# Optimization experiments

Measured on AMD Instinct MI355X. Metric: run time of the kernel, lower is better.

Reference implementation:

```python
import jax, jax.numpy as jnp
import numpy as np

OUTPUT_LEN = 180  # decoder steps, from __init__ default


def gru_cell(x, h, Wih, Whh, bih, bhh):
    """PyTorch-convention GRU cell. x:(B,in) h:(B,H) -> (B,H)."""
    gi = x @ Wih.T + bih          # (B,3H)
    gh = h @ Whh.T + bhh          # (B,3H)
    ir, iz, inn = jnp.split(gi, 3, axis=-1)
    hr, hz, hn = jnp.split(gh, 3, axis=-1)
    r = jax.nn.sigmoid(ir + hr)
    z = jax.nn.sigmoid(iz + hz)
    n = jnp.tanh(inn + r * hn)
    return (1.0 - z) * n + z * h


def setup_inputs() -> dict:
    key = jax.random.key(0)
    B, T_in, N_IN, H = 8192, 512, 2, 64
    ks = jax.random.split(key, 20)
    s = 0.05
    d = {
        "x": jax.random.normal(ks[0], (B, T_in, N_IN), jnp.float32),
        "enc_Wih0": jax.random.normal(ks[1], (3 * H, N_IN), jnp.float32) * s,
        "enc_Whh0": jax.random.normal(ks[2], (3 * H, H), jnp.float32) * s,
        "enc_bih0": jax.random.normal(ks[3], (3 * H,), jnp.float32) * s,
        "enc_bhh0": jax.random.normal(ks[4], (3 * H,), jnp.float32) * s,
        "enc_Wih1": jax.random.normal(ks[5], (3 * H, H), jnp.float32) * s,
        "enc_Whh1": jax.random.normal(ks[6], (3 * H, H), jnp.float32) * s,
        "enc_bih1": jax.random.normal(ks[7], (3 * H,), jnp.float32) * s,
        "enc_bhh1": jax.random.normal(ks[8], (3 * H,), jnp.float32) * s,
        "dec_Wih0": jax.random.normal(ks[9], (3 * H, 1), jnp.float32) * s,
        "dec_Whh0": jax.random.normal(ks[10], (3 * H, H), jnp.float32) * s,
        "dec_bih0": jax.random.normal(ks[11], (3 * H,), jnp.float32) * s,
        "dec_bhh0": jax.random.normal(ks[12], (3 * H,), jnp.float32) * s,
        "dec_Wih1": jax.random.normal(ks[13], (3 * H, H), jnp.float32) * s,
        "dec_Whh1": jax.random.normal(ks[14], (3 * H, H), jnp.float32) * s,
        "dec_bih1": jax.random.normal(ks[15], (3 * H,), jnp.float32) * s,
        "dec_bhh1": jax.random.normal(ks[16], (3 * H,), jnp.float32) * s,
        "out_W": jax.random.normal(ks[17], (1, H), jnp.float32) * s,
        "out_b": jax.random.normal(ks[18], (1,), jnp.float32) * s,
    }
    return d


def reference(x, enc_Wih0, enc_Whh0, enc_bih0, enc_bhh0,
              enc_Wih1, enc_Whh1, enc_bih1, enc_bhh1,
              dec_Wih0, dec_Whh0, dec_bih0, dec_bhh0,
              dec_Wih1, dec_Whh1, dec_bih1, dec_bhh1,
              out_W, out_b):
    B = x.shape[0]
    H = enc_Whh0.shape[1]
    h0 = jnp.zeros((B, H), x.dtype)
    h1 = jnp.zeros((B, H), x.dtype)

    # ---- encoder: 2-layer GRU over input_len steps ----
    def enc_step(carry, xt):
        h0, h1 = carry
        h0 = gru_cell(xt, h0, enc_Wih0, enc_Whh0, enc_bih0, enc_bhh0)
        h1 = gru_cell(h0, h1, enc_Wih1, enc_Whh1, enc_bih1, enc_bhh1)
        return (h0, h1), None

    (h0, h1), _ = jax.lax.scan(enc_step, (h0, h1), jnp.swapaxes(x, 0, 1))

    prev = jnp.zeros((B, 1), x.dtype)

    def dec_step(carry, _):
        h0, h1, prev = carry
        h0 = gru_cell(prev, h0, dec_Wih0, dec_Whh0, dec_bih0, dec_bhh0)
        h1 = gru_cell(h0, h1, dec_Wih1, dec_Whh1, dec_bih1, dec_bhh1)
        cv = h1 @ out_W.T + out_b          # (B,1)
        return (h0, h1, cv), cv

    _, ys = jax.lax.scan(dec_step, (h0, h1, prev), None, length=OUTPUT_LEN)
    # ys: (T, B, 1) -> (B, T, 1)
    return jnp.swapaxes(ys, 0, 1)
```

## Files before the change

kernel.cpp:

```cpp
#include <hip/hip_runtime.h>


typedef __attribute__((ext_vector_type(8))) short bf16x8;
typedef __attribute__((ext_vector_type(4))) float f32x4;

struct Params {
  const float *x;
  const float *wih0e, *bih0e, *bhh0e, *bih1e, *bhh1e;
  const float *wih0d, *bih0d, *bhh0d, *bih1d, *bhh1d;
  const float *outW, *outb;
  const unsigned short *wt;
  float *out;
};

__device__ __forceinline__ float sgm(float v) { return 1.f / (1.f + __expf(-v)); }
__device__ __forceinline__ float th(float v)  { float e = __expf(2.f * v); return 1.f - 2.f / (e + 1.f); }

__device__ __forceinline__ unsigned short rbf(float v) {
  unsigned int u = __float_as_uint(v);
  return (unsigned short)((u + 0x7fffu + ((u >> 16) & 1u)) >> 16);
}
__device__ __forceinline__ float ubf(unsigned short h) {
  return __uint_as_float((unsigned int)h << 16);
}

__device__ __forceinline__ f32x4 mfma16(bf16x8 a, bf16x8 b, f32x4 c) {
  return __builtin_amdgcn_mfma_f32_16x16x32_bf16(a, b, c, 0, 0, 0);
}

__global__ void prep_w(const float* s0, const float* s1, const float* s2,
                       const float* s3, const float* s4, const float* s5,
                       unsigned short* dst) {
  const float* srcs[6] = {s0, s1, s2, s3, s4, s5};
  const float* s = srcs[blockIdx.x];
  unsigned short* o = dst + blockIdx.x * 24576;
  for (int i = threadIdx.x; i < 24576; i += blockDim.x) {
    int e  = i & 7;
    int l  = (i >> 3) & 63;
    int sp = (i >> 9) & 1;
    int kf = (i >> 10) & 1;
    int nt = i >> 11;
    int n = nt * 16 + (l & 15);
    int k = kf * 32 + (l >> 4) * 8 + e;
    float v = s[n * 64 + k];
    unsigned short hi = rbf(v);
    unsigned short val = hi;
    if (sp) val = rbf(v - ubf(hi));
    o[i] = val;
  }
}


__global__ __launch_bounds__(256, 2) void gru_main(Params p) {
  __shared__ unsigned short aH0[2][2048];
  __shared__ unsigned short aH1[2][2048];
  __shared__ float pw[4][16];

  const int tid = threadIdx.x;
  const int l   = tid & 63;
  const int w   = tid >> 6;
  const int jc  = l & 15;
  const int rg  = l >> 4;
  const int j   = w * 16 + jc;
  const int b0  = blockIdx.x * 16;

  const int kfj = j >> 5, rgj = (j >> 3) & 3, ej = j & 7;
  const int wbase = kfj * 1024 + rgj * 128 + ej;
  const int rdb = rg * 128 + ((jc ^ rg) << 3);

  for (int i = tid; i < 2048; i += 256) {
    aH0[0][i] = 0; aH0[1][i] = 0; aH1[0][i] = 0; aH1[1][i] = 0;
  }
  float h0own[4] = {0.f, 0.f, 0.f, 0.f}, h1own[4] = {0.f, 0.f, 0.f, 0.f};

  bf16x8 wB[3][3][2][2];

  for (int ph = 0; ph < 2; ++ph) {
#pragma unroll
    for (int m = 0; m < 3; ++m)
#pragma unroll
      for (int g = 0; g < 3; ++g)
#pragma unroll
        for (int kf = 0; kf < 2; ++kf)
#pragma unroll
          for (int sp = 0; sp < 2; ++sp) {
            int nt = g * 4 + w;
            wB[m][g][kf][sp] = *(const bf16x8*)(p.wt +
                (((((ph * 3 + m) * 12 + nt) * 2 + kf) * 2 + sp) << 9) + l * 8);
          }
    float bi0[3], bh0[3], bi1[3], bh1[3], wxa[3], wxb[3];
#pragma unroll
    for (int g = 0; g < 3; ++g) {
      int r = g * 64 + j;
      if (ph == 0) {
        bi0[g] = p.bih0e[r]; bh0[g] = p.bhh0e[r];
        bi1[g] = p.bih1e[r]; bh1[g] = p.bhh1e[r];
        wxa[g] = p.wih0e[2 * r]; wxb[g] = p.wih0e[2 * r + 1];
      } else {
        bi0[g] = p.bih0d[r]; bh0[g] = p.bhh0d[r];
        bi1[g] = p.bih1d[r]; bh1[g] = p.bhh1d[r];
        wxa[g] = p.wih0d[r]; wxb[g] = 0.f;
      }
    }
    const float oW = p.outW[j], ob = p.outb[0];
    const int T = ph ? 180 : 512;
    __syncthreads();

    for (int t = 0; t < T; ++t) {
#pragma unroll
      for (int m = 0; m < 3; ++m)
#pragma unroll
        for (int g = 0; g < 3; ++g)
#pragma unroll
          for (int kf = 0; kf < 2; ++kf)
#pragma unroll
            for (int sp = 0; sp < 2; ++sp)
              asm volatile("" : "+v"(wB[m][g][kf][sp]));

      const int cur = t & 1;
      float2 xx[4]; float prevv[4];
      if (ph == 0) {
#pragma unroll
        for (int i = 0; i < 4; ++i)
          xx[i] = *(const float2*)(p.x + ((size_t)(b0 + rg * 4 + i) * 512 + t) * 2);
      } else {
        if (t > 0) {
#pragma unroll
          for (int i = 0; i < 4; ++i)
            prevv[i] = ob + pw[0][rg * 4 + i] + pw[1][rg * 4 + i]
                          + pw[2][rg * 4 + i] + pw[3][rg * 4 + i];
          if (w == 0 && jc == 0) {
#pragma unroll
            for (int i = 0; i < 4; ++i)
              p.out[(size_t)(b0 + rg * 4 + i) * 180 + (t - 1)] = prevv[i];
          }
        } else {
#pragma unroll
          for (int i = 0; i < 4; ++i) prevv[i] = 0.f;
        }
      }
      const unsigned short* h0o = aH0[cur ^ 1];
      f32x4 aR = {0,0,0,0}, aZ = {0,0,0,0}, aN = {0,0,0,0};
#pragma unroll
      for (int kf = 0; kf < 2; ++kf) {
        bf16x8 ah = *(const bf16x8*)&h0o[kf * 1024 + rdb];
        bf16x8 al = *(const bf16x8*)&h0o[kf * 1024 + 512 + rdb];
        aR = mfma16(ah, wB[0][0][kf][0], aR);
        aZ = mfma16(ah, wB[0][1][kf][0], aZ);
        aN = mfma16(ah, wB[0][2][kf][0], aN);
        aR = mfma16(al, wB[0][0][kf][0], aR);
        aZ = mfma16(al, wB[0][1][kf][0], aZ);
        aN = mfma16(al, wB[0][2][kf][0], aN);
        aR = mfma16(ah, wB[0][0][kf][1], aR);
        aZ = mfma16(ah, wB[0][1][kf][1], aZ);
        aN = mfma16(ah, wB[0][2][kf][1], aN);
      }
      unsigned short* h0n = aH0[cur];
#pragma unroll
      for (int i = 0; i < 4; ++i) {
        float xr, xz, xn;
        if (ph == 0) {
          xr = bi0[0] + wxa[0] * xx[i].x + wxb[0] * xx[i].y;
          xz = bi0[1] + wxa[1] * xx[i].x + wxb[1] * xx[i].y;
          xn = bi0[2] + wxa[2] * xx[i].x + wxb[2] * xx[i].y;
        } else {
          xr = bi0[0] + wxa[0] * prevv[i];
          xz = bi0[1] + wxa[1] * prevv[i];
          xn = bi0[2] + wxa[2] * prevv[i];
        }
        float r = sgm(xr + bh0[0] + aR[i]);
        float z = sgm(xz + bh0[1] + aZ[i]);
        float n = th(xn + r * (bh0[2] + aN[i]));
        h0own[i] = (1.f - z) * n + z * h0own[i];
        unsigned short hi = rbf(h0own[i]);
        unsigned short lo = rbf(h0own[i] - ubf(hi));
        int idx = wbase + (((rg * 4 + i) ^ rgj) << 3);
        h0n[idx] = hi; h0n[idx + 512] = lo;
      }
      __syncthreads();
      const unsigned short* h1o = aH1[cur ^ 1];
      f32x4 cR = {0,0,0,0}, cZ = {0,0,0,0}, iN = {0,0,0,0}, hN = {0,0,0,0};
#pragma unroll
      for (int kf = 0; kf < 2; ++kf) {
        bf16x8 gh = *(const bf16x8*)&h0n[kf * 1024 + rdb];
        bf16x8 gl = *(const bf16x8*)&h0n[kf * 1024 + 512 + rdb];
        bf16x8 qh = *(const bf16x8*)&h1o[kf * 1024 + rdb];
        bf16x8 ql = *(const bf16x8*)&h1o[kf * 1024 + 512 + rdb];
        cR = mfma16(gh, wB[1][0][kf][0], cR);
        cR = mfma16(qh, wB[2][0][kf][0], cR);
        cZ = mfma16(gh, wB[1][1][kf][0], cZ);
        cZ = mfma16(qh, wB[2][1][kf][0], cZ);
        iN = mfma16(gh, wB[1][2][kf][0], iN);
        hN = mfma16(qh, wB[2][2][kf][0], hN);
        cR = mfma16(gl, wB[1][0][kf][0], cR);
        cR = mfma16(ql, wB[2][0][kf][0], cR);
        cZ = mfma16(gl, wB[1][1][kf][0], cZ);
        cZ = mfma16(ql, wB[2][1][kf][0], cZ);
        iN = mfma16(gl, wB[1][2][kf][0], iN);
        hN = mfma16(ql, wB[2][2][kf][0], hN);
        cR = mfma16(gh, wB[1][0][kf][1], cR);
        cR = mfma16(qh, wB[2][0][kf][1], cR);
        cZ = mfma16(gh, wB[1][1][kf][1], cZ);
        cZ = mfma16(qh, wB[2][1][kf][1], cZ);
        iN = mfma16(gh, wB[1][2][kf][1], iN);
        hN = mfma16(qh, wB[2][2][kf][1], hN);
      }
      unsigned short* h1n = aH1[cur];
      float v[4];
#pragma unroll
      for (int i = 0; i < 4; ++i) {
        float r = sgm(cR[i] + bi1[0] + bh1[0]);
        float z = sgm(cZ[i] + bi1[1] + bh1[1]);
        float n = th(iN[i] + bi1[2] + r * (bh1[2] + hN[i]));
        h1own[i] = (1.f - z) * n + z * h1own[i];
        unsigned short hi = rbf(h1own[i]);
        unsigned short lo = rbf(h1own[i] - ubf(hi));
        int idx = wbase + (((rg * 4 + i) ^ rgj) << 3);
        h1n[idx] = hi; h1n[idx + 512] = lo;
        v[i] = oW * h1own[i];
      }
      if (ph == 1) {
#pragma unroll
        for (int off = 1; off < 16; off <<= 1)
#pragma unroll
          for (int i = 0; i < 4; ++i) v[i] += __shfl_xor(v[i], off, 64);
        if (jc == 0) {
#pragma unroll
          for (int i = 0; i < 4; ++i) pw[w][rg * 4 + i] = v[i];
        }
      }
      __syncthreads();
    }
    if (ph == 1) {
      if (w == 0 && jc == 0) {
#pragma unroll
        for (int i = 0; i < 4; ++i) {
          float fv = ob + pw[0][rg * 4 + i] + pw[1][rg * 4 + i]
                        + pw[2][rg * 4 + i] + pw[3][rg * 4 + i];
          p.out[(size_t)(b0 + rg * 4 + i) * 180 + 179] = fv;
        }
      }
    }
  }
}

extern "C" void kernel_launch(void* const* d_in, const int* in_sizes, int n_in,
                              void* d_out, int out_size, void* d_ws, size_t ws_size,
                              hipStream_t stream) {
  unsigned short* wt = (unsigned short*)d_ws;

  prep_w<<<dim3(6), dim3(256), 0, stream>>>(
      (const float*)d_in[2], (const float*)d_in[5], (const float*)d_in[6],
      (const float*)d_in[10], (const float*)d_in[13], (const float*)d_in[14], wt);

  Params p;
  p.x = (const float*)d_in[0];
  p.wih0e = (const float*)d_in[1];
  p.bih0e = (const float*)d_in[3];
  p.bhh0e = (const float*)d_in[4];
  p.bih1e = (const float*)d_in[7];
  p.bhh1e = (const float*)d_in[8];
  p.wih0d = (const float*)d_in[9];
  p.bih0d = (const float*)d_in[11];
  p.bhh0d = (const float*)d_in[12];
  p.bih1d = (const float*)d_in[15];
  p.bhh1d = (const float*)d_in[16];
  p.outW = (const float*)d_in[17];
  p.outb = (const float*)d_in[18];
  p.wt = wt;
  p.out = (float*)d_out;

  gru_main<<<dim3(512), dim3(256), 0, stream>>>(p);
}
```

Measured before the change: 2.159 ms.

## Process two 16-row batch tiles per block to reuse register-resident weights

Each block now handles 32 batch rows as two 16-row sub-tiles, so the weight fragments held in registers serve twice as many MFMAs. The grid halves to 256 blocks, about one per CU, and the layer-1 recurrent loads are hoisted ahead of the layer-0 MFMAs. The weight fragments are pinned to AGPRs with the "+a" constraint and the occupancy hint is dropped from launch_bounds. The aim is to amortize per-step barriers, LDS traffic and fixed latency over more work and to interleave independent MFMA chains. In exchange it roughly doubles live state per thread and lowers wave occupancy, which may reduce latency hiding.

Measured after the change: 2.534 ms. 17.4% more time.

```diff
diff --git a/kernel.cpp b/kernel.cpp
--- a/kernel.cpp
+++ b/kernel.cpp
@@ -51,10 +51,10 @@
 }
 
 
-__global__ __launch_bounds__(256, 2) void gru_main(Params p) {
-  __shared__ unsigned short aH0[2][2048];
-  __shared__ unsigned short aH1[2][2048];
-  __shared__ float pw[4][16];
+__global__ __launch_bounds__(256) void gru_main(Params p) {
+  __shared__ unsigned short aH0[2 * 4096];
+  __shared__ unsigned short aH1[2 * 4096];
+  __shared__ float pw[4][32];
 
   const int tid = threadIdx.x;
   const int l   = tid & 63;
@@ -62,16 +62,18 @@
   const int jc  = l & 15;
   const int rg  = l >> 4;
   const int j   = w * 16 + jc;
-  const int b0  = blockIdx.x * 16;
+  const int b0  = blockIdx.x * 32;
 
   const int kfj = j >> 5, rgj = (j >> 3) & 3, ej = j & 7;
   const int wbase = kfj * 1024 + rgj * 128 + ej;
   const int rdb = rg * 128 + ((jc ^ rg) << 3);
 
-  for (int i = tid; i < 2048; i += 256) {
-    aH0[0][i] = 0; aH0[1][i] = 0; aH1[0][i] = 0; aH1[1][i] = 0;
-  }
-  float h0own[4] = {0.f, 0.f, 0.f, 0.f}, h1own[4] = {0.f, 0.f, 0.f, 0.f};
+  for (int i = tid; i < 8192; i += 256) { aH0[i] = 0; aH1[i] = 0; }
+  float h0own[2][4], h1own[2][4];
+#pragma unroll
+  for (int rb = 0; rb < 2; ++rb)
+#pragma unroll
+    for (int i = 0; i < 4; ++i) { h0own[rb][i] = 0.f; h1own[rb][i] = 0.f; }
 
   bf16x8 wB[3][3][2][2];
 
@@ -115,118 +117,191 @@
           for (int kf = 0; kf < 2; ++kf)
 #pragma unroll
             for (int sp = 0; sp < 2; ++sp)
-              asm volatile("" : "+v"(wB[m][g][kf][sp]));
+              asm volatile("" : "+a"(wB[m][g][kf][sp]));
 
       const int cur = t & 1;
-      float2 xx[4]; float prevv[4];
+      const unsigned short* h0o = aH0 + (cur ^ 1) * 4096;
+      const unsigned short* h1o = aH1 + (cur ^ 1) * 4096;
+      unsigned short* h0n = aH0 + cur * 4096;
+      unsigned short* h1n = aH1 + cur * 4096;
+
+      float2 xx[2][4]; float prevv[2][4];
       if (ph == 0) {
 #pragma unroll
-        for (int i = 0; i < 4; ++i)
-          xx[i] = *(const float2*)(p.x + ((size_t)(b0 + rg * 4 + i) * 512 + t) * 2);
+        for (int rb = 0; rb < 2; ++rb)
+#pragma unroll
+          for (int i = 0; i < 4; ++i)
+            xx[rb][i] = *(const float2*)(p.x +
+                ((size_t)(b0 + rb * 16 + rg * 4 + i) * 512 + t) * 2);
       } else {
         if (t > 0) {
 #pragma unroll
-          for (int i = 0; i < 4; ++i)
-            prevv[i] = ob + pw[0][rg * 4 + i] + pw[1][rg * 4 + i]
-                          + pw[2][rg * 4 + i] + pw[3][rg * 4 + i];
+          for (int rb = 0; rb < 2; ++rb)
+#pragma unroll
+            for (int i = 0; i < 4; ++i) {
+              int b = rb * 16 + rg * 4 + i;
+              prevv[rb][i] = ob + pw[0][b] + pw[1][b] + pw[2][b] + pw[3][b];
+            }
           if (w == 0 && jc == 0) {
 #pragma unroll
-            for (int i = 0; i < 4; ++i)
-              p.out[(size_t)(b0 + rg * 4 + i) * 180 + (t - 1)] = prevv[i];
+            for (int rb = 0; rb < 2; ++rb)
+#pragma unroll
+              for (int i = 0; i < 4; ++i)
+                p.out[(size_t)(b0 + rb * 16 + rg * 4 + i) * 180 + (t - 1)] =
+                    prevv[rb][i];
           }
         } else {
 #pragma unroll
-          for (int i = 0; i < 4; ++i) prevv[i] = 0.f;
-        }
-      }
-      const unsigned short* h0o = aH0[cur ^ 1];
-      f32x4 aR = {0,0,0,0}, aZ = {0,0,0,0}, aN = {0,0,0,0};
+          for (int rb = 0; rb < 2; ++rb)
+#pragma unroll
+            for (int i = 0; i < 4; ++i) prevv[rb][i] = 0.f;
+        }
+      }
+
+      bf16x8 ah[2][2], al[2][2], qh[2][2], ql[2][2];
+#pragma unroll
+      for (int kf = 0; kf < 2; ++kf)
+#pragma unroll
+        for (int rb = 0; rb < 2; ++rb) {
+          ah[kf][rb] = *(const bf16x8*)&h0o[rb * 2048 + kf * 1024 + rdb];
+          al[kf][rb] = *(const bf16x8*)&h0o[rb * 2048 + kf * 1024 + 512 + rdb];
+          qh[kf][rb] = *(const bf16x8*)&h1o[rb * 2048 + kf * 1024 + rdb];
+          ql[kf][rb] = *(const bf16x8*)&h1o[rb * 2048 + kf * 1024 + 512 + rdb];
+        }
+
+      f32x4 aR[2], aZ[2], aN[2];
+#pragma unroll
+      for (int rb = 0; rb < 2; ++rb) {
+        f32x4 zz = {0.f, 0.f, 0.f, 0.f};
+        aR[rb] = zz; aZ[rb] = zz; aN[rb] = zz;
+      }
 #pragma unroll
       for (int kf = 0; kf < 2; ++kf) {
-        bf16x8 ah = *(const bf16x8*)&h0o[kf * 1024 + rdb];
-        bf16x8 al = *(const bf16x8*)&h0o[kf * 1024 + 512 + rdb];
-        aR = mfma16(ah, wB[0][0][kf][0], aR);
-        aZ = mfma16(ah, wB[0][1][kf][0], aZ);
-        aN = mfma16(ah, wB[0][2][kf][0], aN);
-        aR = mfma16(al, wB[0][0][kf][0], aR);
-        aZ = mfma16(al, wB[0][1][kf][0], aZ);
-        aN = mfma16(al, wB[0][2][kf][0], aN);
-        aR = mfma16(ah, wB[0][0][kf][1], aR);
-        aZ = mfma16(ah, wB[0][1][kf][1], aZ);
-        aN = mfma16(ah, wB[0][2][kf][1], aN);
-      }
-      unsigned short* h0n = aH0[cur];
-#pragma unroll
-      for (int i = 0; i < 4; ++i) {
-        float xr, xz, xn;
-        if (ph == 0) {
-          xr = bi0[0] + wxa[0] * xx[i].x + wxb[0] * xx[i].y;
-          xz = bi0[1] + wxa[1] * xx[i].x + wxb[1] * xx[i].y;
-          xn = bi0[2] + wxa[2] * xx[i].x + wxb[2] * xx[i].y;
-        } else {
-          xr = bi0[0] + wxa[0] * prevv[i];
-          xz = bi0[1] + wxa[1] * prevv[i];
-          xn = bi0[2] + wxa[2] * prevv[i];
-        }
-        float r = sgm(xr + bh0[0] + aR[i]);
-        float z = sgm(xz + bh0[1] + aZ[i]);
-        float n = th(xn + r * (bh0[2] + aN[i]));
-        h0own[i] = (1.f - z) * n + z * h0own[i];
-        unsigned short hi = rbf(h0own[i]);
-        unsigned short lo = rbf(h0own[i] - ubf(hi));
-        int idx = wbase + (((rg * 4 + i) ^ rgj) << 3);
-        h0n[idx] = hi; h0n[idx + 512] = lo;
-      }
+#pragma unroll
+        for (int rb = 0; rb < 2; ++rb) {
+          aR[rb] = mfma16(ah[kf][rb], wB[0][0][kf][0], aR[rb]);
+          aZ[rb] = mfma16(ah[kf][rb], wB[0][1][kf][0], aZ[rb]);
+          aN[rb] = mfma16(ah[kf][rb], wB[0][2][kf][0], aN[rb]);
+        }
+#pragma unroll
+        for (int rb = 0; rb < 2; ++rb) {
+          aR[rb] = mfma16(al[kf][rb], wB[0][0][kf][0], aR[rb]);
+          aZ[rb] = mfma16(al[kf][rb], wB[0][1][kf][0], aZ[rb]);
+          aN[rb] = mfma16(al[kf][rb], wB[0][2][kf][0], aN[rb]);
+        }
+#pragma unroll
+        for (int rb = 0; rb < 2; ++rb) {
+          aR[rb] = mfma16(ah[kf][rb], wB[0][0][kf][1], aR[rb]);
+          aZ[rb] = mfma16(ah[kf][rb], wB[0][1][kf][1], aZ[rb]);
+          aN[rb] = mfma16(ah[kf][rb], wB[0][2][kf][1], aN[rb]);
+        }
+      }
+#pragma unroll
+      for (int rb = 0; rb < 2; ++rb)
+#pragma unroll
+        for (int i = 0; i < 4; ++i) {
+          float xr, xz, xn;
+          if (ph == 0) {
+            xr = bi0[0] + wxa[0] * xx[rb][i].x + wxb[0] * xx[rb][i].y;
+            xz = bi0[1] + wxa[1] * xx[rb][i].x + wxb[1] * xx[rb][i].y;
+            xn = bi0[2] + wxa[2] * xx[rb][i].x + wxb[2] * xx[rb][i].y;
+          } else {
+            xr = bi0[0] + wxa[0] * prevv[rb][i];
+            xz = bi0[1] + wxa[1] * prevv[rb][i];
+            xn = bi0[2] + wxa[2] * prevv[rb][i];
+          }
+          float r = sgm(xr + bh0[0] + aR[rb][i]);
+          float z = sgm(xz + bh0[1] + aZ[rb][i]);
+          float n = th(xn + r * (bh0[2] + aN[rb][i]));
+          h0own[rb][i] = (1.f - z) * n + z * h0own[rb][i];
+          unsigned short hi = rbf(h0own[rb][i]);
+          unsigned short lo = rbf(h0own[rb][i] - ubf(hi));
+          int idx = rb * 2048 + wbase + (((rg * 4 + i) ^ rgj) << 3);
+          h0n[idx] = hi; h0n[idx + 512] = lo;
+        }
       __syncthreads();
-      const unsigned short* h1o = aH1[cur ^ 1];
-      f32x4 cR = {0,0,0,0}, cZ = {0,0,0,0}, iN = {0,0,0,0}, hN = {0,0,0,0};
+      bf16x8 gh[2][2], gl[2][2];
+#pragma unroll
+      for (int kf = 0; kf < 2; ++kf)
+#pragma unroll
+        for (int rb = 0; rb < 2; ++rb) {
+          gh[kf][rb] = *(const bf16x8*)&h0n[rb * 2048 + kf * 1024 + rdb];
+          gl[kf][rb] = *(const bf16x8*)&h0n[rb * 2048 + kf * 1024 + 512 + rdb];
+        }
+      f32x4 cR[2], cZ[2], iN2[2], hN2[2];
+#pragma unroll
+      for (int rb = 0; rb < 2; ++rb) {
+        f32x4 zz = {0.f, 0.f, 0.f, 0.f};
+        cR[rb] = zz; cZ[rb] = zz; iN2[rb] = zz; hN2[rb] = zz;
+      }
 #pragma unroll
       for (int kf = 0; kf < 2; ++kf) {
-        bf16x8 gh = *(const bf16x8*)&h0n[kf * 1024 + rdb];
-        bf16x8 gl = *(const bf16x8*)&h0n[kf * 1024 + 512 + rdb];
-        bf16x8 qh = *(const bf16x8*)&h1o[kf * 1024 + rdb];
-        bf16x8 ql = *(const bf16x8*)&h1o[kf * 1024 + 512 + rdb];
-        cR = mfma16(gh, wB[1][0][kf][0], cR);
-        cR = mfma16(qh, wB[2][0][kf][0], cR);
-        cZ = mfma16(gh, wB[1][1][kf][0], cZ);
-        cZ = mfma16(qh, wB[2][1][kf][0], cZ);
-        iN = mfma16(gh, wB[1][2][kf][0], iN);
-        hN = mfma16(qh, wB[2][2][kf][0], hN);
-        cR = mfma16(gl, wB[1][0][kf][0], cR);
-        cR = mfma16(ql, wB[2][0][kf][0], cR);
-        cZ = mfma16(gl, wB[1][1][kf][0], cZ);
-        cZ = mfma16(ql, wB[2][1][kf][0], cZ);
-        iN = mfma16(gl, wB[1][2][kf][0], iN);
-        hN = mfma16(ql, wB[2][2][kf][0], hN);
-        cR = mfma16(gh, wB[1][0][kf][1], cR);
-        cR = mfma16(qh, wB[2][0][kf][1], cR);
-        cZ = mfma16(gh, wB[1][1][kf][1], cZ);
-        cZ = mfma16(qh, wB[2][1][kf][1], cZ);
-        iN = mfma16(gh, wB[1][2][kf][1], iN);
-        hN = mfma16(qh, wB[2][2][kf][1], hN);
-      }
-      unsigned short* h1n = aH1[cur];
-      float v[4];
-#pragma unroll
-      for (int i = 0; i < 4; ++i) {
-        float r = sgm(cR[i] + bi1[0] + bh1[0]);
-        float z = sgm(cZ[i] + bi1[1] + bh1[1]);
-        float n = th(iN[i] + bi1[2] + r * (bh1[2] + hN[i]));
-        h1own[i] = (1.f - z) * n + z * h1own[i];
-        unsigned short hi = rbf(h1own[i]);
-        unsigned short lo = rbf(h1own[i] - ubf(hi));
-        int idx = wbase + (((rg * 4 + i) ^ rgj) << 3);
-        h1n[idx] = hi; h1n[idx + 512] = lo;
-        v[i] = oW * h1own[i];
-      }
+#pragma unroll
+        for (int rb = 0; rb < 2; ++rb) {
+          cR[rb]  = mfma16(gh[kf][rb], wB[1][0][kf][0], cR[rb]);
+          cZ[rb]  = mfma16(gh[kf][rb], wB[1][1][kf][0], cZ[rb]);
+          iN2[rb] = mfma16(gh[kf][rb], wB[1][2][kf][0], iN2[rb]);
+        }
+#pragma unroll
+        for (int rb = 0; rb < 2; ++rb) {
+          cR[rb]  = mfma16(qh[kf][rb], wB[2][0][kf][0], cR[rb]);
+          cZ[rb]  = mfma16(qh[kf][rb], wB[2][1][kf][0], cZ[rb]);
+          hN2[rb] = mfma16(qh[kf][rb], wB[2][2][kf][0], hN2[rb]);
+        }
+#pragma unroll
+        for (int rb = 0; rb < 2; ++rb) {
+          cR[rb]  = mfma16(gl[kf][rb], wB[1][0][kf][0], cR[rb]);
+          cZ[rb]  = mfma16(gl[kf][rb], wB[1][1][kf][0], cZ[rb]);
+          iN2[rb] = mfma16(gl[kf][rb], wB[1][2][kf][0], iN2[rb]);
+        }
+#pragma unroll
+        for (int rb = 0; rb < 2; ++rb) {
+          cR[rb]  = mfma16(ql[kf][rb], wB[2][0][kf][0], cR[rb]);
+          cZ[rb]  = mfma16(ql[kf][rb], wB[2][1][kf][0], cZ[rb]);
+          hN2[rb] = mfma16(ql[kf][rb], wB[2][2][kf][0], hN2[rb]);
+        }
+#pragma unroll
+        for (int rb = 0; rb < 2; ++rb) {
+          cR[rb]  = mfma16(gh[kf][rb], wB[1][0][kf][1], cR[rb]);
+          cZ[rb]  = mfma16(gh[kf][rb], wB[1][1][kf][1], cZ[rb]);
+          iN2[rb] = mfma16(gh[kf][rb], wB[1][2][kf][1], iN2[rb]);
+        }
+#pragma unroll
+        for (int rb = 0; rb < 2; ++rb) {
+          cR[rb]  = mfma16(qh[kf][rb], wB[2][0][kf][1], cR[rb]);
+          cZ[rb]  = mfma16(qh[kf][rb], wB[2][1][kf][1], cZ[rb]);
+          hN2[rb] = mfma16(qh[kf][rb], wB[2][2][kf][1], hN2[rb]);
+        }
+      }
+      float v[2][4];
+#pragma unroll
+      for (int rb = 0; rb < 2; ++rb)
+#pragma unroll
+        for (int i = 0; i < 4; ++i) {
+          float r = sgm(cR[rb][i] + bi1[0] + bh1[0]);
+          float z = sgm(cZ[rb][i] + bi1[1] + bh1[1]);
+          float n = th(iN2[rb][i] + bi1[2] + r * (bh1[2] + hN2[rb][i]));
+          h1own[rb][i] = (1.f - z) * n + z * h1own[rb][i];
+          unsigned short hi = rbf(h1own[rb][i]);
+          unsigned short lo = rbf(h1own[rb][i] - ubf(hi));
+          int idx = rb * 2048 + wbase + (((rg * 4 + i) ^ rgj) << 3);
+          h1n[idx] = hi; h1n[idx + 512] = lo;
+          v[rb][i] = oW * h1own[rb][i];
+        }
       if (ph == 1) {
 #pragma unroll
         for (int off = 1; off < 16; off <<= 1)
 #pragma unroll
-          for (int i = 0; i < 4; ++i) v[i] += __shfl_xor(v[i], off, 64);
+          for (int rb = 0; rb < 2; ++rb)
+#pragma unroll
+            for (int i = 0; i < 4; ++i)
+              v[rb][i] += __shfl_xor(v[rb][i], off, 64);
         if (jc == 0) {
 #pragma unroll
-          for (int i = 0; i < 4; ++i) pw[w][rg * 4 + i] = v[i];
+          for (int rb = 0; rb < 2; ++rb)
+#pragma unroll
+            for (int i = 0; i < 4; ++i)
+              pw[w][rb * 16 + rg * 4 + i] = v[rb][i];
         }
       }
       __syncthreads();
@@ -234,11 +309,13 @@
     if (ph == 1) {
       if (w == 0 && jc == 0) {
 #pragma unroll
-        for (int i = 0; i < 4; ++i) {
-          float fv = ob + pw[0][rg * 4 + i] + pw[1][rg * 4 + i]
-                        + pw[2][rg * 4 + i] + pw[3][rg * 4 + i];
-          p.out[(size_t)(b0 + rg * 4 + i) * 180 + 179] = fv;
-        }
+        for (int rb = 0; rb < 2; ++rb)
+#pragma unroll
+          for (int i = 0; i < 4; ++i) {
+            int b = rb * 16 + rg * 4 + i;
+            float fv = ob + pw[0][b] + pw[1][b] + pw[2][b] + pw[3][b];
+            p.out[(size_t)(b0 + b) * 180 + 179] = fv;
+          }
       }
     }
   }
@@ -270,5 +347,5 @@
   p.wt = wt;
   p.out = (float*)d_out;
 
-  gru_main<<<dim3(512), dim3(256), 0, stream>>>(p);
-}
+  gru_main<<<dim3(256), dim3(256), 0, stream>>>(p);
+}
```

## Stream layer-0 weights per step, pin layer-1 weights in AGPRs, hoist LDS reads

Applied to the files above, without the earlier changes.

Layer-0 recurrent weight fragments are no longer held in registers for the whole phase. They are reloaded from global memory (likely L1/L2 hits) every timestep, which cuts the resident weight register footprint by a third. The layer-1 weight fragments are now constrained to accumulator registers (AGPRs) via the asm constraint, freeing VGPRs. The previous-step h0/h1 LDS reads are hoisted ahead of the first MFMA chain and the MFMA order is interleaved. This trades extra global/cache traffic on the serial critical path for lower register pressure and possibly better scheduling.

After: 2.467 ms. +14.3%, slower.

```diff
diff --git a/kernel.cpp b/kernel.cpp
--- a/kernel.cpp
+++ b/kernel.cpp
@@ -73,11 +73,12 @@
   }
   float h0own[4] = {0.f, 0.f, 0.f, 0.f}, h1own[4] = {0.f, 0.f, 0.f, 0.f};
 
-  bf16x8 wB[3][3][2][2];
+  bf16x8 wB1[2][3][2][2];
 
   for (int ph = 0; ph < 2; ++ph) {
-#pragma unroll
-    for (int m = 0; m < 3; ++m)
+    const unsigned short* wt0 = p.wt + (ph * 3) * 24576;
+#pragma unroll
+    for (int m = 0; m < 2; ++m)
 #pragma unroll
       for (int g = 0; g < 3; ++g)
 #pragma unroll
@@ -85,8 +86,8 @@
 #pragma unroll
           for (int sp = 0; sp < 2; ++sp) {
             int nt = g * 4 + w;
-            wB[m][g][kf][sp] = *(const bf16x8*)(p.wt +
-                (((((ph * 3 + m) * 12 + nt) * 2 + kf) * 2 + sp) << 9) + l * 8);
+            wB1[m][g][kf][sp] = *(const bf16x8*)(p.wt +
+                (((((ph * 3 + 1 + m) * 12 + nt) * 2 + kf) * 2 + sp) << 9) + l * 8);
           }
     float bi0[3], bh0[3], bi1[3], bh1[3], wxa[3], wxb[3];
 #pragma unroll
@@ -108,16 +109,21 @@
 
     for (int t = 0; t < T; ++t) {
 #pragma unroll
-      for (int m = 0; m < 3; ++m)
+      for (int m = 0; m < 2; ++m)
 #pragma unroll
         for (int g = 0; g < 3; ++g)
 #pragma unroll
           for (int kf = 0; kf < 2; ++kf)
 #pragma unroll
             for (int sp = 0; sp < 2; ++sp)
-              asm volatile("" : "+v"(wB[m][g][kf][sp]));
+              asm volatile("" : "+a"(wB1[m][g][kf][sp]));
 
       const int cur = t & 1;
+      const unsigned short* h0o = aH0[cur ^ 1];
+      const unsigned short* h1o = aH1[cur ^ 1];
+      unsigned short* h0n = aH0[cur];
+      unsigned short* h1n = aH1[cur];
+
       float2 xx[4]; float prevv[4];
       if (ph == 0) {
 #pragma unroll
@@ -139,23 +145,38 @@
           for (int i = 0; i < 4; ++i) prevv[i] = 0.f;
         }
       }
-      const unsigned short* h0o = aH0[cur ^ 1];
+
+      bf16x8 w0[3][2][2];
+#pragma unroll
+      for (int g = 0; g < 3; ++g)
+#pragma unroll
+        for (int kf = 0; kf < 2; ++kf)
+#pragma unroll
+          for (int sp = 0; sp < 2; ++sp)
+            w0[g][kf][sp] = *(const bf16x8*)(wt0 +
+                ((((g * 4 + w) * 2 + kf) * 2 + sp) << 9) + l * 8);
+
+      bf16x8 ah[2], al[2], qh[2], ql[2];
+#pragma unroll
+      for (int kf = 0; kf < 2; ++kf) {
+        ah[kf] = *(const bf16x8*)&h0o[kf * 1024 + rdb];
+        al[kf] = *(const bf16x8*)&h0o[kf * 1024 + 512 + rdb];
+        qh[kf] = *(const bf16x8*)&h1o[kf * 1024 + rdb];
+        ql[kf] = *(const bf16x8*)&h1o[kf * 1024 + 512 + rdb];
+      }
       f32x4 aR = {0,0,0,0}, aZ = {0,0,0,0}, aN = {0,0,0,0};
 #pragma unroll
       for (int kf = 0; kf < 2; ++kf) {
-        bf16x8 ah = *(const bf16x8*)&h0o[kf * 1024 + rdb];
-        bf16x8 al = *(const bf16x8*)&h0o[kf * 1024 + 512 + rdb];
-        aR = mfma16(ah, wB[0][0][kf][0], aR);
-        aZ = mfma16(ah, wB[0][1][kf][0], aZ);
-        aN = mfma16(ah, wB[0][2][kf][0], aN);
-        aR = mfma16(al, wB[0][0][kf][0], aR);
-        aZ = mfma16(al, wB[0][1][kf][0], aZ);
-        aN = mfma16(al, wB[0][2][kf][0], aN);
-        aR = mfma16(ah, wB[0][0][kf][1], aR);
-        aZ = mfma16(ah, wB[0][1][kf][1], aZ);
-        aN = mfma16(ah, wB[0][2][kf][1], aN);
-      }
-      unsigned short* h0n = aH0[cur];
+        aR = mfma16(ah[kf], w0[0][kf][0], aR);
+        aZ = mfma16(ah[kf], w0[1][kf][0], aZ);
+        aN = mfma16(ah[kf], w0[2][kf][0], aN);
+        aR = mfma16(al[kf], w0[0][kf][0], aR);
+        aZ = mfma16(al[kf], w0[1][kf][0], aZ);
+        aN = mfma16(al[kf], w0[2][kf][0], aN);
+        aR = mfma16(ah[kf], w0[0][kf][1], aR);
+        aZ = mfma16(ah[kf], w0[1][kf][1], aZ);
+        aN = mfma16(ah[kf], w0[2][kf][1], aN);
+      }
 #pragma unroll
       for (int i = 0; i < 4; ++i) {
         float xr, xz, xn;
@@ -178,34 +199,34 @@
         h0n[idx] = hi; h0n[idx + 512] = lo;
       }
       __syncthreads();
-      const unsigned short* h1o = aH1[cur ^ 1];
+      bf16x8 gh[2], gl[2];
+#pragma unroll
+      for (int kf = 0; kf < 2; ++kf) {
+        gh[kf] = *(const bf16x8*)&h0n[kf * 1024 + rdb];
+        gl[kf] = *(const bf16x8*)&h0n[kf * 1024 + 512 + rdb];
+      }
       f32x4 cR = {0,0,0,0}, cZ = {0,0,0,0}, iN = {0,0,0,0}, hN = {0,0,0,0};
 #pragma unroll
       for (int kf = 0; kf < 2; ++kf) {
-        bf16x8 gh = *(const bf16x8*)&h0n[kf * 1024 + rdb];
-        bf16x8 gl = *(const bf16x8*)&h0n[kf * 1024 + 512 + rdb];
-        bf16x8 qh = *(const bf16x8*)&h1o[kf * 1024 + rdb];
-        bf16x8 ql = *(const bf16x8*)&h1o[kf * 1024 + 512 + rdb];
-        cR = mfma16(gh, wB[1][0][kf][0], cR);
-        cR = mfma16(qh, wB[2][0][kf][0], cR);
-        cZ = mfma16(gh, wB[1][1][kf][0], cZ);
-        cZ = mfma16(qh, wB[2][1][kf][0], cZ);
-        iN = mfma16(gh, wB[1][2][kf][0], iN);
-        hN = mfma16(qh, wB[2][2][kf][0], hN);
-        cR = mfma16(gl, wB[1][0][kf][0], cR);
-        cR = mfma16(ql, wB[2][0][kf][0], cR);
-        cZ = mfma16(gl, wB[1][1][kf][0], cZ);
-        cZ = mfma16(ql, wB[2][1][kf][0], cZ);
-        iN = mfma16(gl, wB[1][2][kf][0], iN);
-        hN = mfma16(ql, wB[2][2][kf][0], hN);
-        cR = mfma16(gh, wB[1][0][kf][1], cR);
-        cR = mfma16(qh, wB[2][0][kf][1], cR);
-        cZ = mfma16(gh, wB[1][1][kf][1], cZ);
-        cZ = mfma16(qh, wB[2][1][kf][1], cZ);
-        iN = mfma16(gh, wB[1][2][kf][1], iN);
-        hN = mfma16(qh, wB[2][2][kf][1], hN);
-      }
-      unsigned short* h1n = aH1[cur];
+        cR = mfma16(gh[kf], wB1[0][0][kf][0], cR);
+        cZ = mfma16(gh[kf], wB1[0][1][kf][0], cZ);
+        iN = mfma16(gh[kf], wB1[0][2][kf][0], iN);
+        cR = mfma16(qh[kf], wB1[1][0][kf][0], cR);
+        cZ = mfma16(qh[kf], wB1[1][1][kf][0], cZ);
+        hN = mfma16(qh[kf], wB1[1][2][kf][0], hN);
+        cR = mfma16(gl[kf], wB1[0][0][kf][0], cR);
+        cZ = mfma16(gl[kf], wB1[0][1][kf][0], cZ);
+        iN = mfma16(gl[kf], wB1[0][2][kf][0], iN);
+        cR = mfma16(ql[kf], wB1[1][0][kf][0], cR);
+        cZ = mfma16(ql[kf], wB1[1][1][kf][0], cZ);
+        hN = mfma16(ql[kf], wB1[1][2][kf][0], hN);
+        cR = mfma16(gh[kf], wB1[0][0][kf][1], cR);
+        cZ = mfma16(gh[kf], wB1[0][1][kf][1], cZ);
+        iN = mfma16(gh[kf], wB1[0][2][kf][1], iN);
+        cR = mfma16(qh[kf], wB1[1][0][kf][1], cR);
+        cZ = mfma16(qh[kf], wB1[1][1][kf][1], cZ);
+        hN = mfma16(qh[kf], wB1[1][2][kf][1], hN);
+      }
       float v[4];
 #pragma unroll
       for (int i = 0; i < 4; ++i) {
```
